# Kernel optimization log

Hardware: AMD Instinct MI355X
Metric: run time of the kernel (lower is better)

## Reference

```python
import jax, jax.numpy as jnp
import numpy as np

B, S, D_MODEL, H, D_HEAD = 4, 2048, 1024, 16, 64
SCALE = D_HEAD ** -0.5


def setup_inputs() -> dict:
    key = jax.random.key(0)
    ks = jax.random.split(key, 6)
    init = lambda k, shp: jax.random.normal(k, shp, jnp.float32) * (shp[0] ** -0.5)
    Xq = jax.random.normal(ks[0], (B, S, D_MODEL), jnp.float32)
    # pre-softmax bool mask: True = masked (fill -inf) -> causal
    mask_bef = jnp.triu(jnp.ones((S, S), dtype=bool), k=1)
    # post-softmax bool mask: True = zero out that attention weight
    mask_aft = jax.random.bernoulli(ks[1], 0.1, (S, S))
    Wq = init(ks[2], (D_MODEL, H * D_HEAD))
    Wk = init(ks[3], (D_MODEL, H * D_HEAD))
    Wv = init(ks[4], (D_MODEL, H * D_HEAD))
    Wo = init(ks[5], (H * D_HEAD, D_MODEL))
    return {"Xq": Xq, "mask_bef": mask_bef, "mask_aft": mask_aft,
            "Wq": Wq, "Wk": Wk, "Wv": Wv, "Wo": Wo}


def reference(Xq, mask_bef, mask_aft, Wq, Wk, Wv, Wo):
    # Self-attention: Xk = Xv = Xq
    def split_heads(X, W):  # [B,S,D] @ [D,H*d] -> [B,H,S,d]
        return (X @ W).reshape(B, S, H, D_HEAD).transpose(0, 2, 1, 3)

    Q = split_heads(Xq, Wq)
    K = split_heads(Xq, Wk)
    V = split_heads(Xq, Wv)
    # scores: [B,H,Sq,Sk]
    scores = jnp.einsum('bhqd,bhkd->bhqk', Q, K) * SCALE
    scores = jnp.where(mask_bef, -jnp.inf, scores)  # pre-softmax bool mask
    attn = jax.nn.softmax(scores, axis=-1)
    attn = jnp.where(mask_aft, 0.0, attn)           # post-softmax bool mask
    out = jnp.einsum('bhqk,bhkd->bhqd', attn, V)    # [B,H,S,d]
    out = out.transpose(0, 2, 1, 3).reshape(B, S, H * D_HEAD)
    return out @ Wo  # [B,S,out_dim_o]
```

## Files before the change

### kernel.cpp

```cpp
#include <hip/hip_runtime.h>
#include <hip/hip_bf16.h>


using bf16 = __hip_bfloat16;
typedef __attribute__((ext_vector_type(8))) short short8;
typedef __attribute__((ext_vector_type(4))) float floatx4;

#define kB 4
#define kS 2048
#define kDM 1024
#define kH 16
#define kDH 64
#define kHeadElems ((size_t)kB * kH * kS * kDH)
#define STR 72

#if __has_builtin(__builtin_amdgcn_exp2f)
#define EXP2(x) __builtin_amdgcn_exp2f(x)
#else
#define EXP2(x) __expf((x) * 0.69314718056f)
#endif

__device__ __forceinline__ unsigned short f2bf(float f) {
    union { float f; unsigned u; } x{f};
    unsigned r = x.u + 0x7fff + ((x.u >> 16) & 1);
    return (unsigned short)(r >> 16);
}
__device__ __forceinline__ unsigned cvt_pk_bf16(float lo, float hi) {
    unsigned r;
    asm("v_cvt_pk_bf16_f32 %0, %1, %2" : "=v"(r) : "v"(lo), "v"(hi));
    return r;
}
__device__ __forceinline__ void gl_lds16(const void* g, void* l) {
    __builtin_amdgcn_global_load_lds(
        (const __attribute__((address_space(1))) unsigned int*)g,
        (__attribute__((address_space(3))) unsigned int*)l, 16, 0, 0);
}

__global__ __launch_bounds__(256)
void pack_em(const int* __restrict__ mask_aft, unsigned short* __restrict__ EM)
{
    const size_t i = ((size_t)blockIdx.x * 256 + threadIdx.x) * 8;
    const int q  = (int)(i >> 11);
    const int k0 = (int)(i & 2047);
    const int4 m0 = *(const int4*)(mask_aft + i);
    const int4 m1 = *(const int4*)(mask_aft + i + 4);
    union { unsigned short u[8]; uint4 v; } o;
    o.u[0] = (m0.x || (k0 + 0) > q) ? 0 : 0xFFFFu;
    o.u[1] = (m0.y || (k0 + 1) > q) ? 0 : 0xFFFFu;
    o.u[2] = (m0.z || (k0 + 2) > q) ? 0 : 0xFFFFu;
    o.u[3] = (m0.w || (k0 + 3) > q) ? 0 : 0xFFFFu;
    o.u[4] = (m1.x || (k0 + 4) > q) ? 0 : 0xFFFFu;
    o.u[5] = (m1.y || (k0 + 5) > q) ? 0 : 0xFFFFu;
    o.u[6] = (m1.z || (k0 + 6) > q) ? 0 : 0xFFFFu;
    o.u[7] = (m1.w || (k0 + 7) > q) ? 0 : 0xFFFFu;
    *(uint4*)(EM + i) = o.v;
}

__global__ __launch_bounds__(256)
void conv_x(const float* __restrict__ X, bf16* __restrict__ Xb)
{
    const size_t i = ((size_t)blockIdx.x * 256 + threadIdx.x) * 8;
    const float4 a = *(const float4*)(X + i);
    const float4 b = *(const float4*)(X + i + 4);
    union { unsigned short u[8]; uint4 v; } o;
    o.u[0] = f2bf(a.x); o.u[1] = f2bf(a.y); o.u[2] = f2bf(a.z); o.u[3] = f2bf(a.w);
    o.u[4] = f2bf(b.x); o.u[5] = f2bf(b.y); o.u[6] = f2bf(b.z); o.u[7] = f2bf(b.w);
    *(uint4*)(Xb + i) = o.v;
}

__global__ __launch_bounds__(256)
void conv_wT(const float* __restrict__ W, bf16* __restrict__ WT)
{
    __shared__ unsigned short Ls[64][STR];
    const int k0 = blockIdx.x * 64, n0 = blockIdx.y * 64;
    const int tid = threadIdx.x;
    const int r16 = tid >> 4, c4 = (tid & 15) * 4;
    #pragma unroll
    for (int it = 0; it < 4; ++it) {
        const int r = it * 16 + r16;
        const float4 v = *(const float4*)(W + (size_t)(k0 + r) * kDM + n0 + c4);
        Ls[c4 + 0][r] = f2bf(v.x); Ls[c4 + 1][r] = f2bf(v.y);
        Ls[c4 + 2][r] = f2bf(v.z); Ls[c4 + 3][r] = f2bf(v.w);
    }
    __syncthreads();
    #pragma unroll
    for (int it = 0; it < 4; ++it) {
        const int rn = it * 16 + r16;
        ushort4 u;
        u.x = Ls[rn][c4 + 0]; u.y = Ls[rn][c4 + 1];
        u.z = Ls[rn][c4 + 2]; u.w = Ls[rn][c4 + 3];
        *(ushort4*)(WT + (size_t)(n0 + rn) * kDM + k0 + c4) = u;
    }
}

__global__ __launch_bounds__(256)
void qkv_mfma(const bf16* __restrict__ A, const bf16* __restrict__ BT,
              bf16* __restrict__ ws)
{
    __shared__ __align__(16) unsigned short At[128][32];
    __shared__ __align__(16) unsigned short Bt[128][32];
    const int tid = threadIdx.x;
    const int w = tid >> 6, lane = tid & 63;
    const int quad = (tid >> 4) & 3, col = tid & 15;
    const int wm = w >> 1, wn = w & 1;
    const int flat = blockIdx.x + blockIdx.y * 24;
    const int xcd = flat & 7;
    const int i2 = flat >> 3;
    const int n0 = (xcd * 3 + (i2 % 3)) * 128;
    const int m0 = (i2 / 3) * 128;

    const bf16* pA = A  + (size_t)(m0 + w * 32 + (lane >> 2)) * kDM + (lane & 3) * 8;
    const bf16* pB = BT + (size_t)(n0 + w * 32 + (lane >> 2)) * kDM + (lane & 3) * 8;
    unsigned short* lA = &At[w * 32][0];
    unsigned short* lB = &Bt[w * 32][0];

    floatx4 acc[4][4];
    #pragma unroll
    for (int i = 0; i < 4; ++i)
        #pragma unroll
        for (int j = 0; j < 4; ++j) acc[i][j] = (floatx4){0.f, 0.f, 0.f, 0.f};

    for (int k0 = 0; k0 < kDM; k0 += 32) {
        __syncthreads();
        gl_lds16(pA + k0, lA);
        gl_lds16(pA + k0 + 16 * kDM, lA + 16 * 32);
        gl_lds16(pB + k0, lB);
        gl_lds16(pB + k0 + 16 * kDM, lB + 16 * 32);
        __syncthreads();
        short8 aA[4], bB[4];
        #pragma unroll
        for (int i = 0; i < 4; ++i)
            aA[i] = *(const short8*)&At[wm * 64 + i * 16 + col][quad * 8];
        #pragma unroll
        for (int j = 0; j < 4; ++j)
            bB[j] = *(const short8*)&Bt[wn * 64 + j * 16 + col][quad * 8];
        #pragma unroll
        for (int i = 0; i < 4; ++i)
            #pragma unroll
            for (int j = 0; j < 4; ++j)
                acc[i][j] = __builtin_amdgcn_mfma_f32_16x16x32_bf16(aA[i], bB[j], acc[i][j], 0, 0, 0);
    }

    const int p  = n0 >> 10;
    const int nn = n0 & 1023;
    const float scl = (p == 0) ? 0.18033688f : 1.0f;
    bf16* Out = ws + (size_t)p * kHeadElems;
    #pragma unroll
    for (int i = 0; i < 4; ++i) {
        #pragma unroll
        for (int r = 0; r < 4; ++r) {
            const int m = m0 + wm * 64 + i * 16 + quad * 4 + r;
            const int b = m >> 11, s = m & 2047;
            #pragma unroll
            for (int j = 0; j < 4; ++j) {
                const int n = nn + wn * 64 + j * 16 + col;
                const int h = n >> 6, d = n & 63;
                Out[((size_t)(b * kH + h) * kS + s) * kDH + d] = __float2bfloat16(acc[i][j][r] * scl);
            }
        }
    }
}

__global__ __launch_bounds__(256)
void vtrans(const bf16* __restrict__ V, bf16* __restrict__ VT)
{
    const int bh = blockIdx.y;
    const int s0 = blockIdx.x * 64;
    const bf16* src = V + (size_t)bh * kS * kDH;
    bf16* dst = VT + (size_t)bh * kS * kDH;
    __shared__ unsigned short L[64][STR];
    const int tid = threadIdx.x;
    #pragma unroll
    for (int t = 0; t < 2; ++t) {
        const int idx = t * 256 + tid;
        const int r = idx >> 3, c8 = (idx & 7) * 8;
        *(uint4*)&L[r][c8] = *(const uint4*)(src + (size_t)(s0 + r) * kDH + c8);
    }
    __syncthreads();
    #pragma unroll
    for (int t = 0; t < 2; ++t) {
        const int idx = t * 256 + tid;
        const int d = idx >> 3, sc = (idx & 7) * 8;
        unsigned short tmp[8];
        #pragma unroll
        for (int e = 0; e < 8; ++e) tmp[e] = L[sc + e][d];
        *(uint4*)(dst + (size_t)d * kS + s0 + sc) = *(uint4*)tmp;
    }
}

__global__ __launch_bounds__(256, 3)
void attn_mfma(const bf16* __restrict__ ws, const bf16* __restrict__ VT,
               const unsigned short* __restrict__ EM,
               bf16* __restrict__ Aout)
{
    const int flat = blockIdx.x + blockIdx.y * 16;
    const int xcd = flat & 7;
    const int idx = flat >> 3;
    const int bh  = xcd * 8 + (idx & 7);
    const int j   = idx >> 3;
    const int kk  = 3 - (j >> 2);
    const int qtile = 4 * kk + ((kk + (j & 3)) & 3);
    const int q0 = qtile * 128;

    const int b = bh >> 4, h = bh & 15;
    const int tid  = threadIdx.x;
    const int w    = tid >> 6;
    const int lane = tid & 63;
    const int quad = (tid >> 4) & 3;
    const int col  = tid & 15;

    const size_t ho = (size_t)bh * kS * kDH;
    const bf16* Qg  = ws + ho;
    const bf16* Kg  = ws + kHeadElems + ho;
    const bf16* VTg = VT + ho;

    __shared__ __align__(16) unsigned short Ks[2][64][64];
    __shared__ __align__(16) unsigned short Vs[2][64][64];
    __shared__ __align__(16) unsigned short Pw[4][2][16][STR];

    const int qw = q0 + w * 32;
    const int swz = col & 7;
    const int sch = (lane & 7) ^ (lane >> 3);

    short8 bQ[2][2];
    const unsigned short* EMq[2];
    #pragma unroll
    for (int sub = 0; sub < 2; ++sub) {
        const bf16* qrow = Qg + (size_t)(qw + sub * 16 + col) * kDH;
        bQ[sub][0] = *(const short8*)(qrow + quad * 8);
        bQ[sub][1] = *(const short8*)(qrow + 32 + quad * 8);
        EMq[sub] = EM + (size_t)(qw + sub * 16 + col) * kS;
    }

    floatx4 Ov[2][4];
    #pragma unroll
    for (int sub = 0; sub < 2; ++sub)
        #pragma unroll
        for (int dg = 0; dg < 4; ++dg) Ov[sub][dg] = (floatx4){0.f, 0.f, 0.f, 0.f};
    float lacc[2] = {0.f, 0.f};

    const int nt = qtile * 2 + 2;

    auto STAGE = [&](int buf, int kt) {
        const bf16* Kt = Kg  + (size_t)(kt * 64) * kDH;
        const bf16* Vt = VTg + kt * 64;
        #pragma unroll
        for (int t = 0; t < 2; ++t) {
            const int rbase = (t * 4 + w) * 8;
            const int r = rbase + (lane >> 3);
            gl_lds16(Kt + (size_t)r * kDH + sch * 8, &Ks[buf][rbase][0]);
            gl_lds16(Vt + (size_t)r * kS  + sch * 8, &Vs[buf][rbase][0]);
        }
    };

    STAGE(0, 0);
    asm volatile("s_waitcnt vmcnt(0)" ::: "memory");
    __builtin_amdgcn_s_barrier();
    __builtin_amdgcn_sched_barrier(0);

    int cur = 0;
    for (int kt = 0; kt < nt; ++kt) {
        const int kt64 = kt * 64;
        const bool doC = (kt64 <= qw + 31);

        uint2 em[2][4];
        if (doC) {
            #pragma unroll
            for (int sub = 0; sub < 2; ++sub)
                #pragma unroll
                for (int g = 0; g < 4; ++g)
                    em[sub][g] = *(const uint2*)(EMq[sub] + kt64 + g * 16 + quad * 4);
            __builtin_amdgcn_sched_barrier(0);
        }

        if (kt + 1 < nt) STAGE(cur ^ 1, kt + 1);

        if (doC) {
            floatx4 sg[2][4];
            __builtin_amdgcn_s_setprio(1);
            #pragma unroll
            for (int g = 0; g < 4; ++g) {
                const int krow = g * 16 + col;
                const short8 aK0 = *(const short8*)&Ks[cur][krow][(quad ^ swz) * 8];
                const short8 aK1 = *(const short8*)&Ks[cur][krow][((4 + quad) ^ swz) * 8];
                floatx4 sA = {0.f, 0.f, 0.f, 0.f}, sB = {0.f, 0.f, 0.f, 0.f};
                sA = __builtin_amdgcn_mfma_f32_16x16x32_bf16(aK0, bQ[0][0], sA, 0, 0, 0);
                sA = __builtin_amdgcn_mfma_f32_16x16x32_bf16(aK1, bQ[0][1], sA, 0, 0, 0);
                sB = __builtin_amdgcn_mfma_f32_16x16x32_bf16(aK0, bQ[1][0], sB, 0, 0, 0);
                sB = __builtin_amdgcn_mfma_f32_16x16x32_bf16(aK1, bQ[1][1], sB, 0, 0, 0);
                sg[0][g] = sA; sg[1][g] = sB;
            }
            __builtin_amdgcn_s_setprio(0);

            #pragma unroll
            for (int sub = 0; sub < 2; ++sub) {
                const int qbase = qw + sub * 16;
                const bool needC = (kt64 + 63 > qbase);
                float lc = 0.f;
                #pragma unroll
                for (int g = 0; g < 4; ++g) {
                    const float p0 = EXP2(sg[sub][g][0]);
                    const float p1 = EXP2(sg[sub][g][1]);
                    const float p2 = EXP2(sg[sub][g][2]);
                    const float p3 = EXP2(sg[sub][g][3]);
                    if (needC) {
                        const int kb = kt64 + g * 16 + quad * 4;
                        const int qme = qbase + col;
                        lc += (kb + 0 <= qme) ? p0 : 0.f;
                        lc += (kb + 1 <= qme) ? p1 : 0.f;
                        lc += (kb + 2 <= qme) ? p2 : 0.f;
                        lc += (kb + 3 <= qme) ? p3 : 0.f;
                    } else {
                        lc += (p0 + p1) + (p2 + p3);
                    }
                    uint2 pk;
                    pk.x = cvt_pk_bf16(p0, p1) & em[sub][g].x;
                    pk.y = cvt_pk_bf16(p2, p3) & em[sub][g].y;
                    *(uint2*)&Pw[w][sub][col][g * 16 + quad * 4] = pk;
                }
                lacc[sub] += lc;
            }

            const short8 aP[2][2] = {
                { *(const short8*)&Pw[w][0][col][quad * 8],
                  *(const short8*)&Pw[w][0][col][32 + quad * 8] },
                { *(const short8*)&Pw[w][1][col][quad * 8],
                  *(const short8*)&Pw[w][1][col][32 + quad * 8] } };
            __builtin_amdgcn_s_setprio(1);
            #pragma unroll
            for (int dg = 0; dg < 4; ++dg) {
                const int vrow = dg * 16 + col;
                const short8 bV0 = *(const short8*)&Vs[cur][vrow][(quad ^ swz) * 8];
                const short8 bV1 = *(const short8*)&Vs[cur][vrow][((4 + quad) ^ swz) * 8];
                Ov[0][dg] = __builtin_amdgcn_mfma_f32_16x16x32_bf16(aP[0][0], bV0, Ov[0][dg], 0, 0, 0);
                Ov[0][dg] = __builtin_amdgcn_mfma_f32_16x16x32_bf16(aP[0][1], bV1, Ov[0][dg], 0, 0, 0);
                Ov[1][dg] = __builtin_amdgcn_mfma_f32_16x16x32_bf16(aP[1][0], bV0, Ov[1][dg], 0, 0, 0);
                Ov[1][dg] = __builtin_amdgcn_mfma_f32_16x16x32_bf16(aP[1][1], bV1, Ov[1][dg], 0, 0, 0);
            }
            __builtin_amdgcn_s_setprio(0);
        }

        asm volatile("s_waitcnt vmcnt(0)" ::: "memory");
        __builtin_amdgcn_s_barrier();
        __builtin_amdgcn_sched_barrier(0);
        cur ^= 1;
    }

    #pragma unroll
    for (int sub = 0; sub < 2; ++sub) {
        float l = lacc[sub];
        l += __shfl_xor(l, 16, 64);
        l += __shfl_xor(l, 32, 64);
        const float linv = 1.f / l;
        #pragma unroll
        for (int r = 0; r < 4; ++r) {
            const float sc = __shfl(linv, quad * 4 + r, 64);
            const int q = qw + sub * 16 + quad * 4 + r;
            bf16* orow = Aout + ((size_t)(b * kS + q)) * kDM + h * kDH;
            #pragma unroll
            for (int dg = 0; dg < 4; ++dg)
                orow[dg * 16 + col] = __float2bfloat16(Ov[sub][dg][r] * sc);
        }
    }
}

__global__ __launch_bounds__(256)
void out_mfma(const bf16* __restrict__ A, const bf16* __restrict__ BT,
              float* __restrict__ Out)
{
    __shared__ __align__(16) unsigned short At[128][32];
    __shared__ __align__(16) unsigned short Bt[128][32];
    const int tid = threadIdx.x;
    const int w = tid >> 6, lane = tid & 63;
    const int quad = (tid >> 4) & 3, col = tid & 15;
    const int wm = w >> 1, wn = w & 1;
    const int flat = blockIdx.x + blockIdx.y * 8;
    const int n0 = (flat & 7) * 128;
    const int m0 = (flat >> 3) * 128;

    const bf16* pA = A  + (size_t)(m0 + w * 32 + (lane >> 2)) * kDM + (lane & 3) * 8;
    const bf16* pB = BT + (size_t)(n0 + w * 32 + (lane >> 2)) * kDM + (lane & 3) * 8;
    unsigned short* lA = &At[w * 32][0];
    unsigned short* lB = &Bt[w * 32][0];

    floatx4 acc[4][4];
    #pragma unroll
    for (int i = 0; i < 4; ++i)
        #pragma unroll
        for (int j = 0; j < 4; ++j) acc[i][j] = (floatx4){0.f, 0.f, 0.f, 0.f};

    for (int k0 = 0; k0 < kDM; k0 += 32) {
        __syncthreads();
        gl_lds16(pA + k0, lA);
        gl_lds16(pA + k0 + 16 * kDM, lA + 16 * 32);
        gl_lds16(pB + k0, lB);
        gl_lds16(pB + k0 + 16 * kDM, lB + 16 * 32);
        __syncthreads();
        short8 aA[4], bB[4];
        #pragma unroll
        for (int i = 0; i < 4; ++i)
            aA[i] = *(const short8*)&At[wm * 64 + i * 16 + col][quad * 8];
        #pragma unroll
        for (int j = 0; j < 4; ++j)
            bB[j] = *(const short8*)&Bt[wn * 64 + j * 16 + col][quad * 8];
        #pragma unroll
        for (int i = 0; i < 4; ++i)
            #pragma unroll
            for (int j = 0; j < 4; ++j)
                acc[i][j] = __builtin_amdgcn_mfma_f32_16x16x32_bf16(aA[i], bB[j], acc[i][j], 0, 0, 0);
    }

    #pragma unroll
    for (int i = 0; i < 4; ++i)
        #pragma unroll
        for (int r = 0; r < 4; ++r) {
            const int m = m0 + wm * 64 + i * 16 + quad * 4 + r;
            #pragma unroll
            for (int j = 0; j < 4; ++j)
                Out[(size_t)m * kDM + n0 + wn * 64 + j * 16 + col] = acc[i][j][r];
        }
}

extern "C" void kernel_launch(void* const* d_in, const int* in_sizes, int n_in,
                              void* d_out, int out_size, void* d_ws, size_t ws_size,
                              hipStream_t stream)
{
    const float* Xq       = (const float*)d_in[0];
    const int*   mask_aft = (const int*)d_in[2];
    const float* Wq       = (const float*)d_in[3];
    const float* Wk       = (const float*)d_in[4];
    const float* Wv       = (const float*)d_in[5];
    const float* Wo       = (const float*)d_in[6];
    float* out = (float*)d_out;

    bf16* ws   = (bf16*)d_ws;
    bf16* Xbf  = ws + 3 * kHeadElems;
    bf16* Aout = Xbf;
    bf16* WoT  = ws;

    bf16* WcatT = (bf16*)d_out + 262144;
    bf16* VT    = (bf16*)((char*)d_out + 8u * 1024 * 1024);
    unsigned short* EMp = (unsigned short*)((char*)d_out + 24u * 1024 * 1024);

    pack_em <<<dim3(2048), 256, 0, stream>>>(mask_aft, EMp);
    conv_x  <<<dim3(4096), 256, 0, stream>>>(Xq, Xbf);
    conv_wT <<<dim3(16, 16), 256, 0, stream>>>(Wq, WcatT);
    conv_wT <<<dim3(16, 16), 256, 0, stream>>>(Wk, WcatT + (size_t)kDM * kDM);
    conv_wT <<<dim3(16, 16), 256, 0, stream>>>(Wv, WcatT + 2 * (size_t)kDM * kDM);
    qkv_mfma<<<dim3(24, 64), 256, 0, stream>>>(Xbf, WcatT, ws);
    vtrans  <<<dim3(32, 64), 256, 0, stream>>>(ws + 2 * kHeadElems, VT);
    attn_mfma<<<dim3(16, 64), 256, 0, stream>>>(ws, VT, EMp, Aout);
    conv_wT <<<dim3(16, 16), 256, 0, stream>>>(Wo, WoT);
    out_mfma<<<dim3(8, 64), 256, 0, stream>>>(Aout, WoT, out);
}
```

Before: 323.9 us.

## Fuse preprocessing launches, shrink P scratch with XOR swizzle, raise attention occupancy

```diff
diff --git a/kernel.cpp b/kernel.cpp
--- a/kernel.cpp
+++ b/kernel.cpp
@@ -37,35 +37,63 @@
 }
 
 __global__ __launch_bounds__(256)
-void pack_em(const int* __restrict__ mask_aft, unsigned short* __restrict__ EM)
-{
-    const size_t i = ((size_t)blockIdx.x * 256 + threadIdx.x) * 8;
-    const int q  = (int)(i >> 11);
-    const int k0 = (int)(i & 2047);
-    const int4 m0 = *(const int4*)(mask_aft + i);
-    const int4 m1 = *(const int4*)(mask_aft + i + 4);
-    union { unsigned short u[8]; uint4 v; } o;
-    o.u[0] = (m0.x || (k0 + 0) > q) ? 0 : 0xFFFFu;
-    o.u[1] = (m0.y || (k0 + 1) > q) ? 0 : 0xFFFFu;
-    o.u[2] = (m0.z || (k0 + 2) > q) ? 0 : 0xFFFFu;
-    o.u[3] = (m0.w || (k0 + 3) > q) ? 0 : 0xFFFFu;
-    o.u[4] = (m1.x || (k0 + 4) > q) ? 0 : 0xFFFFu;
-    o.u[5] = (m1.y || (k0 + 5) > q) ? 0 : 0xFFFFu;
-    o.u[6] = (m1.z || (k0 + 6) > q) ? 0 : 0xFFFFu;
-    o.u[7] = (m1.w || (k0 + 7) > q) ? 0 : 0xFFFFu;
-    *(uint4*)(EM + i) = o.v;
-}
-
-__global__ __launch_bounds__(256)
-void conv_x(const float* __restrict__ X, bf16* __restrict__ Xb)
-{
-    const size_t i = ((size_t)blockIdx.x * 256 + threadIdx.x) * 8;
-    const float4 a = *(const float4*)(X + i);
-    const float4 b = *(const float4*)(X + i + 4);
-    union { unsigned short u[8]; uint4 v; } o;
-    o.u[0] = f2bf(a.x); o.u[1] = f2bf(a.y); o.u[2] = f2bf(a.z); o.u[3] = f2bf(a.w);
-    o.u[4] = f2bf(b.x); o.u[5] = f2bf(b.y); o.u[6] = f2bf(b.z); o.u[7] = f2bf(b.w);
-    *(uint4*)(Xb + i) = o.v;
+void fused_pre(const float* __restrict__ X, bf16* __restrict__ Xb,
+               const int* __restrict__ mask_aft, unsigned short* __restrict__ EM)
+{
+    const int bid = blockIdx.x;
+    if (bid < 4096) {
+        const size_t i = ((size_t)bid * 256 + threadIdx.x) * 8;
+        const float4 a = *(const float4*)(X + i);
+        const float4 b = *(const float4*)(X + i + 4);
+        union { unsigned short u[8]; uint4 v; } o;
+        o.u[0] = f2bf(a.x); o.u[1] = f2bf(a.y); o.u[2] = f2bf(a.z); o.u[3] = f2bf(a.w);
+        o.u[4] = f2bf(b.x); o.u[5] = f2bf(b.y); o.u[6] = f2bf(b.z); o.u[7] = f2bf(b.w);
+        *(uint4*)(Xb + i) = o.v;
+    } else {
+        const size_t i = ((size_t)(bid - 4096) * 256 + threadIdx.x) * 8;
+        const int q  = (int)(i >> 11);
+        const int k0 = (int)(i & 2047);
+        const int4 m0 = *(const int4*)(mask_aft + i);
+        const int4 m1 = *(const int4*)(mask_aft + i + 4);
+        union { unsigned short u[8]; uint4 v; } o;
+        o.u[0] = (m0.x || (k0 + 0) > q) ? 0 : 0xFFFFu;
+        o.u[1] = (m0.y || (k0 + 1) > q) ? 0 : 0xFFFFu;
+        o.u[2] = (m0.z || (k0 + 2) > q) ? 0 : 0xFFFFu;
+        o.u[3] = (m0.w || (k0 + 3) > q) ? 0 : 0xFFFFu;
+        o.u[4] = (m1.x || (k0 + 4) > q) ? 0 : 0xFFFFu;
+        o.u[5] = (m1.y || (k0 + 5) > q) ? 0 : 0xFFFFu;
+        o.u[6] = (m1.z || (k0 + 6) > q) ? 0 : 0xFFFFu;
+        o.u[7] = (m1.w || (k0 + 7) > q) ? 0 : 0xFFFFu;
+        *(uint4*)(EM + i) = o.v;
+    }
+}
+
+__global__ __launch_bounds__(256)
+void conv_w3(const float* __restrict__ Wq, const float* __restrict__ Wk,
+             const float* __restrict__ Wv, bf16* __restrict__ WT)
+{
+    const float* W = (blockIdx.z == 0) ? Wq : (blockIdx.z == 1) ? Wk : Wv;
+    bf16* dst = WT + (size_t)blockIdx.z * kDM * kDM;
+    __shared__ unsigned short Ls[64][STR];
+    const int k0 = blockIdx.x * 64, n0 = blockIdx.y * 64;
+    const int tid = threadIdx.x;
+    const int r16 = tid >> 4, c4 = (tid & 15) * 4;
+    #pragma unroll
+    for (int it = 0; it < 4; ++it) {
+        const int r = it * 16 + r16;
+        const float4 v = *(const float4*)(W + (size_t)(k0 + r) * kDM + n0 + c4);
+        Ls[c4 + 0][r] = f2bf(v.x); Ls[c4 + 1][r] = f2bf(v.y);
+        Ls[c4 + 2][r] = f2bf(v.z); Ls[c4 + 3][r] = f2bf(v.w);
+    }
+    __syncthreads();
+    #pragma unroll
+    for (int it = 0; it < 4; ++it) {
+        const int rn = it * 16 + r16;
+        ushort4 u;
+        u.x = Ls[rn][c4 + 0]; u.y = Ls[rn][c4 + 1];
+        u.z = Ls[rn][c4 + 2]; u.w = Ls[rn][c4 + 3];
+        *(ushort4*)(dst + (size_t)(n0 + rn) * kDM + k0 + c4) = u;
+    }
 }
 
 __global__ __launch_bounds__(256)
@@ -188,7 +216,7 @@
     }
 }
 
-__global__ __launch_bounds__(256, 3)
+__global__ __launch_bounds__(256, 4)
 void attn_mfma(const bf16* __restrict__ ws, const bf16* __restrict__ VT,
                const unsigned short* __restrict__ EM,
                bf16* __restrict__ Aout)
@@ -216,11 +244,13 @@
 
     __shared__ __align__(16) unsigned short Ks[2][64][64];
     __shared__ __align__(16) unsigned short Vs[2][64][64];
-    __shared__ __align__(16) unsigned short Pw[4][2][16][STR];
+    __shared__ __align__(16) unsigned short Pw[4][16][64];
 
     const int qw = q0 + w * 32;
     const int swz = col & 7;
     const int sch = (lane & 7) ^ (lane >> 3);
+    const unsigned pswz = (unsigned)(col & 7) << 4;
+    char* PwB = (char*)&Pw[w][col][0];
 
     short8 bQ[2][2];
     const unsigned short* EMq[2];
@@ -292,6 +322,7 @@
             }
             __builtin_amdgcn_s_setprio(0);
 
+            short8 aP[2][2];
             #pragma unroll
             for (int sub = 0; sub < 2; ++sub) {
                 const int qbase = qw + sub * 16;
@@ -316,16 +347,13 @@
                     uint2 pk;
                     pk.x = cvt_pk_bf16(p0, p1) & em[sub][g].x;
                     pk.y = cvt_pk_bf16(p2, p3) & em[sub][g].y;
-                    *(uint2*)&Pw[w][sub][col][g * 16 + quad * 4] = pk;
+                    *(uint2*)(PwB + (((unsigned)(g * 32 + quad * 8)) ^ pswz)) = pk;
                 }
                 lacc[sub] += lc;
+                aP[sub][0] = *(const short8*)(PwB + (((unsigned)(quad * 16)) ^ pswz));
+                aP[sub][1] = *(const short8*)(PwB + (((unsigned)(64 + quad * 16)) ^ pswz));
             }
 
-            const short8 aP[2][2] = {
-                { *(const short8*)&Pw[w][0][col][quad * 8],
-                  *(const short8*)&Pw[w][0][col][32 + quad * 8] },
-                { *(const short8*)&Pw[w][1][col][quad * 8],
-                  *(const short8*)&Pw[w][1][col][32 + quad * 8] } };
             __builtin_amdgcn_s_setprio(1);
             #pragma unroll
             for (int dg = 0; dg < 4; ++dg) {
@@ -442,11 +470,8 @@
     bf16* VT    = (bf16*)((char*)d_out + 8u * 1024 * 1024);
     unsigned short* EMp = (unsigned short*)((char*)d_out + 24u * 1024 * 1024);
 
-    pack_em <<<dim3(2048), 256, 0, stream>>>(mask_aft, EMp);
-    conv_x  <<<dim3(4096), 256, 0, stream>>>(Xq, Xbf);
-    conv_wT <<<dim3(16, 16), 256, 0, stream>>>(Wq, WcatT);
-    conv_wT <<<dim3(16, 16), 256, 0, stream>>>(Wk, WcatT + (size_t)kDM * kDM);
-    conv_wT <<<dim3(16, 16), 256, 0, stream>>>(Wv, WcatT + 2 * (size_t)kDM * kDM);
+    fused_pre<<<dim3(6144), 256, 0, stream>>>(Xq, Xbf, mask_aft, EMp);
+    conv_w3 <<<dim3(16, 16, 3), 256, 0, stream>>>(Wq, Wk, Wv, WcatT);
     qkv_mfma<<<dim3(24, 64), 256, 0, stream>>>(Xbf, WcatT, ws);
     vtrans  <<<dim3(32, 64), 256, 0, stream>>>(ws + 2 * kHeadElems, VT);
     attn_mfma<<<dim3(16, 64), 256, 0, stream>>>(ws, VT, EMp, Aout);
```

After: 371.6 us. 14.7% more time.
